# Kernel optimization log

Hardware: AMD Instinct MI355X
Metric: run time of the kernel (lower is better)

Reference implementation:

```python
import jax, jax.numpy as jnp
import numpy as np

V_PATCH = (1, 2, 4, 8, 16, 32)
RESI = 0.5   # abs(quant_resi)
BETA = 0.25
K_PHI = 4    # share_quant_resi


def _phi_idx(si, SN, K=K_PHI):
    # PhiPartiallyShared.__getitem__ with at = si/(SN-1)
    ticks = np.linspace(1/3/K, 1 - 1/3/K, K) if K == 4 else np.linspace(1/2/K, 1 - 1/2/K, K)
    return int(np.argmin(np.abs(ticks - si / (SN - 1))))


def _area_down(x, pn):
    # F.interpolate mode='area' with pn | H  == exact block mean
    B, C, H, W = x.shape
    return x.reshape(B, C, pn, H // pn, pn, W // pn).mean(axis=(3, 5))


def _bilinear(x, size):
    # matches torch bilinear, align_corners=False, antialias=False (half-pixel centers)
    B, C, _, _ = x.shape
    return jax.image.resize(x, (B, C, size, size), method='bilinear', antialias=False)


def _down(x, pn, si):
    if pn == x.shape[2]:
        return x
    return _area_down(x, pn) if si <= 3 else _bilinear(x, pn)


def _phi_ada(h, w, b, fw, fb, sn):
    # Phi_ada: conv weight modulated by fc(SN); fc is zero-init but kept in the graph
    C = h.shape[1]
    cond = (fw[:, 0] * jnp.float32(sn) + fb).reshape(C, C, 1, 1)
    wmod = w * (1.0 + cond)
    y = jax.lax.conv_general_dilated(h, wmod, (1, 1), 'SAME',
                                     dimension_numbers=('NCHW', 'OIHW', 'NCHW'))
    y = y + b[None, :, None, None]
    return h * (1.0 - RESI) + y * RESI


def _forward(f, embed_w, conv_w, conv_b, fc_w, fc_b):
    B, C, H, W = f.shape
    SN = len(V_PATCH)
    f_ng = jax.lax.stop_gradient(f)
    f_rest = f_ng
    f_hat = jnp.zeros_like(f_ng)
    e_ng = jax.lax.stop_gradient(embed_w)            # embedding.weight.data
    e_sq = jnp.sum(e_ng * e_ng, axis=1)              # [V]
    vq_losses = []
    commit = jnp.float32(0.0)
    for si, pn in enumerate(V_PATCH):
        rest = f_rest if si == SN - 1 else _down(f_rest, pn, si)
        rest_NC = rest.transpose(0, 2, 3, 1).reshape(-1, C)          # [N,C]
        # squared L2 distances to codebook, argmin (non-differentiable)
        d = (jnp.sum(rest_NC * rest_NC, axis=1, keepdims=True)
             + e_sq - 2.0 * (rest_NC @ e_ng.T))                       # [N,V]
        idx = jnp.argmin(d, axis=1)                                   # [N]
        h = embed_w[idx].reshape(B, pn, pn, C).transpose(0, 3, 1, 2)  # [B,C,pn,pn]
        if si != SN - 1:
            h = _bilinear(h, H)
        k = _phi_idx(si, SN)
        h = _phi_ada(h, conv_w[k], conv_b[k], fc_w[k], fc_b[k], SN)
        f_hat = f_hat + h
        f_rest = f_rest - jax.lax.stop_gradient(h)    # grad through f_rest is killed by argmin anyway
        vq_losses.append(jnp.mean((f_hat - f_ng) ** 2))
        fh_ng = jax.lax.stop_gradient(f_hat)
        commit = commit + jnp.mean((_down(fh_ng, pn, si) - _down(f, pn, si)) ** 2) * BETA
    commit = commit / SN
    # straight-through estimator
    f_hat_out = jax.lax.stop_gradient(f_hat) - f_ng + f
    return f_hat_out, jnp.stack(vq_losses), commit


def setup_inputs() -> dict:
    key = jax.random.key(0)
    k1, k2, k3 = jax.random.split(key, 3)
    B, C, H, W = 32, 64, 32, 32
    V = 4096
    f_BChw = jax.random.normal(k1, (B, C, H, W), dtype=jnp.float32)
    embed_w = jax.random.normal(k2, (V, C), dtype=jnp.float32) * 0.5  # trunc_normal std=0.5
    conv_w = jax.random.normal(k3, (K_PHI, C, C, 3, 3), dtype=jnp.float32) * 0.02
    conv_b = jnp.zeros((K_PHI, C), dtype=jnp.float32)
    fc_w = jnp.zeros((K_PHI, C * C, 1), dtype=jnp.float32)  # Phi_ada.fc zero-init
    fc_b = jnp.zeros((K_PHI, C * C), dtype=jnp.float32)
    return {'f_BChw': f_BChw, 'embed_w': embed_w, 'conv_w': conv_w,
            'conv_b': conv_b, 'fc_w': fc_w, 'fc_b': fc_b}


def reference(f_BChw, embed_w, conv_w, conv_b, fc_w, fc_b):
    return _forward(f_BChw, embed_w, conv_w, conv_b, fc_w, fc_b)
```

## Files before the change

### kernel.cpp

```cpp
#include <hip/hip_runtime.h>
#include <cfloat>

#define N_ELEM 2097152
#define TAU 2.0e-2f

typedef short s16x8 __attribute__((ext_vector_type(8)));
typedef float f32x4 __attribute__((ext_vector_type(4)));

__device__ __forceinline__ unsigned short f2bf(float v) {
    unsigned u = __float_as_uint(v);
    u += 0x7FFFu + ((u >> 16) & 1u);
    return (unsigned short)(u >> 16);
}
__device__ __forceinline__ float bf2f(unsigned short h) {
    return __uint_as_float(((unsigned)h) << 16);
}

__device__ __forceinline__ float blockReduceSum(float v) {
    __shared__ float red[4];
    #pragma unroll
    for (int off = 32; off; off >>= 1) v += __shfl_down(v, off, 64);
    int wid = threadIdx.x >> 6, lane = threadIdx.x & 63;
    if (lane == 0) red[wid] = v;
    __syncthreads();
    float r = 0.f;
    if (threadIdx.x == 0) {
        int nw = ((int)blockDim.x + 63) >> 6;
        for (int w = 0; w < nw; ++w) r += red[w];
    }
    __syncthreads();
    return r;
}

__global__ void k_embprep(const float* __restrict__ e, float* __restrict__ hesq,
                          unsigned short* __restrict__ ehiN, unsigned short* __restrict__ eloN) {
    int v = blockIdx.x * 256 + threadIdx.x;
    if (v >= 4096) return;
    const float4* r = (const float4*)(e + (size_t)v * 64);
    float s = 0.f;
    #pragma unroll
    for (int i = 0; i < 16; ++i) {
        float4 a = r[i];
        s += a.x * a.x + a.y * a.y + a.z * a.z + a.w * a.w;
    }
    hesq[v] = 0.5f * s;
    for (int i = 0; i < 64; ++i) {
        float x = e[(size_t)v * 64 + i];
        unsigned short h = f2bf(x);
        ehiN[(size_t)v * 64 + i] = h ^ 0x8000u;
        eloN[(size_t)v * 64 + i] = f2bf(x - bf2f(h)) ^ 0x8000u;
    }
}

__global__ void k_wmod(const float* __restrict__ w, const float* __restrict__ fcw,
                       const float* __restrict__ fcb,
                       unsigned short* __restrict__ wh, unsigned short* __restrict__ wl) {
    int i = blockIdx.x * 256 + threadIdx.x;
    if (i >= 4 * 64 * 64 * 9) return;
    int k = i / (64 * 64 * 9);
    int r = i % (64 * 64 * 9);
    int oi = r / 9;
    int t = r % 9;
    int co = oi >> 6, ci = oi & 63;
    float cond = fcw[k * 4096 + oi] * 6.0f + fcb[k * 4096 + oi];
    float v = w[i] * (1.0f + cond);
    size_t o = ((size_t)(k * 9 + t) * 64 + co) * 64 + ci;
    unsigned short h = f2bf(v);
    wh[o] = h;
    wl[o] = f2bf(v - bf2f(h));
}

__global__ __launch_bounds__(256) void k_down_plane(
        const float* __restrict__ f, const float* __restrict__ fhat,
        float* __restrict__ restnc, unsigned short* __restrict__ dhi,
        unsigned short* __restrict__ dlo, float* __restrict__ cmpPrev, int pn) {
    __shared__ float hs[32][16];
    __shared__ float cr[32][16];
    __shared__ float pm[256];
    int bc = blockIdx.x;
    int c = bc & 63, b = bc >> 6;
    int t = threadIdx.x;
    const float4* fp = (const float4*)(f + (size_t)bc * 1024);
    const float4* hp = (const float4*)(fhat + (size_t)bc * 1024);
    float4 a = fp[t], q = hp[t];
    int r = t >> 3, c4 = t & 7;
    hs[r][c4 * 2]     = (a.x - q.x) + (a.y - q.y);
    hs[r][c4 * 2 + 1] = (a.z - q.z) + (a.w - q.w);
    __syncthreads();
    int cpp = 16 / pn;
    for (int i = t; i < 32 * pn; i += 256) {
        int rr = i / pn, px = i % pn;
        float s = 0.f;
        for (int j = 0; j < cpp; ++j) s += hs[rr][px * cpp + j];
        cr[rr][px] = s;
    }
    __syncthreads();
    int s_ = 32 / pn;
    float inv = 1.0f / (float)(s_ * s_);
    for (int p = t; p < pn * pn; p += 256) {
        int py = p / pn, px = p % pn;
        float s = 0.f;
        for (int j = 0; j < s_; ++j) s += cr[py * s_ + j][px];
        float m = s * inv;
        pm[p] = m;
        int n = (b * pn + py) * pn + px;
        size_t o = (size_t)n * 64 + c;
        unsigned short h = f2bf(m);
        restnc[o] = m;
        dhi[o] = h;
        dlo[o] = f2bf(m - bf2f(h));
    }
    if (pn >= 2) {
        __syncthreads();
        int pnp = pn >> 1;
        float m2 = 0.f;
        for (int p = t; p < pnp * pnp; p += 256) {
            int py = p / pnp, px = p % pnp;
            float mm = 0.25f * (pm[(2 * py) * pn + 2 * px] + pm[(2 * py) * pn + 2 * px + 1]
                              + pm[(2 * py + 1) * pn + 2 * px] + pm[(2 * py + 1) * pn + 2 * px + 1]);
            m2 += mm * mm;
        }
        m2 = blockReduceSum(m2);
        if (t == 0) cmpPrev[blockIdx.x] = m2;
    }
}

__global__ void k_trans_nc(const float* __restrict__ A, const float* __restrict__ Bt,
                           float* __restrict__ dst,
                           unsigned short* __restrict__ dhi, unsigned short* __restrict__ dlo) {
    __shared__ float t[64][65];
    int b = blockIdx.x;
    int p0 = blockIdx.y * 64;
    int lane = threadIdx.x & 63, r4 = threadIdx.x >> 6;
    #pragma unroll
    for (int i = 0; i < 16; ++i) {
        int c = i * 4 + r4;
        size_t g = ((size_t)b * 64 + c) * 1024 + p0 + lane;
        t[c][lane] = A[g] - Bt[g];
    }
    __syncthreads();
    #pragma unroll
    for (int i = 0; i < 16; ++i) {
        int p = i * 4 + r4;
        size_t o = ((size_t)(b * 1024 + p0 + p)) * 64 + lane;
        float v = t[lane][p];
        unsigned short h = f2bf(v);
        dst[o] = v;
        dhi[o] = h;
        dlo[o] = f2bf(v - bf2f(h));
    }
}

__global__ __launch_bounds__(256) void k_commit_rest(const float* __restrict__ restnc,
                                                     float* __restrict__ cmp) {
    int i = blockIdx.x * 256 + threadIdx.x;
    int c = i & 63;
    int p = i >> 6;
    int px = p & 15; p >>= 4;
    int py = p & 15; p >>= 4;
    int b = p;
    int n00 = (b * 32 + 2 * py) * 32 + 2 * px;
    float m = 0.25f * (restnc[(size_t)n00 * 64 + c] + restnc[(size_t)(n00 + 1) * 64 + c]
                     + restnc[(size_t)(n00 + 32) * 64 + c] + restnc[(size_t)(n00 + 33) * 64 + c]);
    float m2 = blockReduceSum(m * m);
    if (threadIdx.x == 0) cmp[blockIdx.x] = m2;
}

__global__ __launch_bounds__(256) void k_vq_mfma(
        const unsigned short* __restrict__ resthi, const unsigned short* __restrict__ restlo,
        const unsigned short* __restrict__ embhiN, const unsigned short* __restrict__ embloN,
        const float* __restrict__ hesq,
        float* __restrict__ m1v_, int* __restrict__ m1i_, float* __restrict__ m2v_,
        int N, int CPS) {
    __shared__ __align__(16) unsigned short lah[64 * 64];
    __shared__ __align__(16) unsigned short lal[64 * 64];
    __shared__ __align__(16) float lq[64];
    int tid = threadIdx.x;
    int lane = tid & 63, wv = tid >> 6;
    int split = blockIdx.y;
    int p0 = blockIdx.x * 128 + wv * 32;
    int cr = lane & 15, oct = lane >> 4;
    int ko8 = oct * 8;
    int ptA = p0 + cr, ptB = p0 + 16 + cr;
    int pA = min(ptA, N - 1), pB = min(ptB, N - 1);

    const unsigned short* ra = resthi + (size_t)pA * 64;
    const unsigned short* la = restlo + (size_t)pA * 64;
    const unsigned short* rb = resthi + (size_t)pB * 64;
    const unsigned short* lb = restlo + (size_t)pB * 64;
    s16x8 bhA0 = *(const s16x8*)(ra + ko8);
    s16x8 bhA1 = *(const s16x8*)(ra + 32 + ko8);
    s16x8 blA0 = *(const s16x8*)(la + ko8);
    s16x8 blA1 = *(const s16x8*)(la + 32 + ko8);
    s16x8 bhB0 = *(const s16x8*)(rb + ko8);
    s16x8 bhB1 = *(const s16x8*)(rb + 32 + ko8);
    s16x8 blB0 = *(const s16x8*)(lb + ko8);
    s16x8 blB1 = *(const s16x8*)(lb + 32 + ko8);

    float m1vA = FLT_MAX, m2vA = FLT_MAX; int m1iA = 0;
    float m1vB = FLT_MAX, m2vB = FLT_MAX; int m1iB = 0;

    int cbeg = split * CPS;
    for (int oc = 0; oc < CPS; oc += 64) {
        int cb = cbeg + oc;
        __syncthreads();
        for (int t = tid; t < 512; t += 256) {
            int cc = t >> 3, part = t & 7;
            int bo = (cc * 128 + part * 16) ^ ((cc & 7) << 4);
            *(uint4*)((char*)lah + bo) = *(const uint4*)(embhiN + (size_t)(cb + cc) * 64 + part * 8);
            *(uint4*)((char*)lal + bo) = *(const uint4*)(embloN + (size_t)(cb + cc) * 64 + part * 8);
        }
        if (tid < 64) lq[tid] = hesq[cb + tid];
        __syncthreads();
        #pragma unroll
        for (int sub = 0; sub < 4; ++sub) {
            int cl = sub * 16 + cr;
            int sw = (cl & 7) << 4;
            int rowb = cl * 128;
            s16x8 ah0 = *(const s16x8*)((const char*)lah + ((rowb + ko8 * 2) ^ sw));
            s16x8 ah1 = *(const s16x8*)((const char*)lah + ((rowb + 64 + ko8 * 2) ^ sw));
            s16x8 al0 = *(const s16x8*)((const char*)lal + ((rowb + ko8 * 2) ^ sw));
            s16x8 al1 = *(const s16x8*)((const char*)lal + ((rowb + 64 + ko8 * 2) ^ sw));
            f32x4 q = *(const f32x4*)(lq + sub * 16 + oct * 4);
            int crow = cb + sub * 16 + oct * 4;
            f32x4 acc = q;
            acc = __builtin_amdgcn_mfma_f32_16x16x32_bf16(ah0, bhA0, acc, 0, 0, 0);
            acc = __builtin_amdgcn_mfma_f32_16x16x32_bf16(ah1, bhA1, acc, 0, 0, 0);
            acc = __builtin_amdgcn_mfma_f32_16x16x32_bf16(ah0, blA0, acc, 0, 0, 0);
            acc = __builtin_amdgcn_mfma_f32_16x16x32_bf16(ah1, blA1, acc, 0, 0, 0);
            acc = __builtin_amdgcn_mfma_f32_16x16x32_bf16(al0, bhA0, acc, 0, 0, 0);
            acc = __builtin_amdgcn_mfma_f32_16x16x32_bf16(al1, bhA1, acc, 0, 0, 0);
            #pragma unroll
            for (int r = 0; r < 4; ++r) {
                float s = acc[r]; int c = crow + r;
                bool lt1 = s < m1vA, lt2 = s < m2vA;
                float nm2 = lt2 ? s : m2vA;
                m2vA = lt1 ? m1vA : nm2;
                m1iA = lt1 ? c : m1iA;
                m1vA = lt1 ? s : m1vA;
            }
            f32x4 accB = q;
            accB = __builtin_amdgcn_mfma_f32_16x16x32_bf16(ah0, bhB0, accB, 0, 0, 0);
            accB = __builtin_amdgcn_mfma_f32_16x16x32_bf16(ah1, bhB1, accB, 0, 0, 0);
            accB = __builtin_amdgcn_mfma_f32_16x16x32_bf16(ah0, blB0, accB, 0, 0, 0);
            accB = __builtin_amdgcn_mfma_f32_16x16x32_bf16(ah1, blB1, accB, 0, 0, 0);
            accB = __builtin_amdgcn_mfma_f32_16x16x32_bf16(al0, bhB0, accB, 0, 0, 0);
            accB = __builtin_amdgcn_mfma_f32_16x16x32_bf16(al1, bhB1, accB, 0, 0, 0);
            #pragma unroll
            for (int r = 0; r < 4; ++r) {
                float s = accB[r]; int c = crow + r;
                bool lt1 = s < m1vB, lt2 = s < m2vB;
                float nm2 = lt2 ? s : m2vB;
                m2vB = lt1 ? m1vB : nm2;
                m1iB = lt1 ? c : m1iB;
                m1vB = lt1 ? s : m1vB;
            }
        }
    }
    #pragma unroll
    for (int off = 16; off <= 32; off <<= 1) {
        float o1 = __shfl_xor(m1vA, off, 64); int oi = __shfl_xor(m1iA, off, 64);
        float o2 = __shfl_xor(m2vA, off, 64);
        if (o1 < m1vA) { m2vA = fminf(m1vA, o2); m1vA = o1; m1iA = oi; }
        else if (o1 < m2vA) m2vA = o1;
        o1 = __shfl_xor(m1vB, off, 64); oi = __shfl_xor(m1iB, off, 64);
        o2 = __shfl_xor(m2vB, off, 64);
        if (o1 < m1vB) { m2vB = fminf(m1vB, o2); m1vB = o1; m1iB = oi; }
        else if (o1 < m2vB) m2vB = o1;
    }
    if (oct == 0) {
        if (ptA < N) { size_t o = (size_t)split * N + ptA; m1v_[o] = m1vA; m1i_[o] = m1iA; m2v_[o] = m2vA; }
        if (ptB < N) { size_t o = (size_t)split * N + ptB; m1v_[o] = m1vB; m1i_[o] = m1iB; m2v_[o] = m2vB; }
    }
}

__global__ void k_vq_combine(const float* __restrict__ m1v_, const int* __restrict__ m1i_,
                             const float* __restrict__ m2v_,
                             int* __restrict__ idx, int* __restrict__ flag, int* __restrict__ count,
                             unsigned long long* __restrict__ pmin, int N, int SPLITS) {
    int n = blockIdx.x * 256 + threadIdx.x;
    if (n >= N) return;
    float a1v = m1v_[n], a2v = m2v_[n];
    int a1i = m1i_[n];
    for (int s = 1; s < SPLITS; ++s) {
        size_t o = (size_t)s * N + n;
        float b1v = m1v_[o], b2v = m2v_[o];
        int b1i = m1i_[o];
        if (b1v < a1v) {
            a2v = fminf(a1v, b2v);
            a1v = b1v; a1i = b1i;
        } else if (b1v < a2v) {
            a2v = b1v;
        }
    }
    idx[n] = a1i;
    pmin[n] = 0xFFFFFFFFFFFFFFFFull;
    if (a2v - a1v < TAU) {
        int p = atomicAdd(count, 1);
        flag[p] = n;
    }
}

__global__ __launch_bounds__(256) void k_vq_exact(
        const float* __restrict__ restnc, const float* __restrict__ embed,
        const float* __restrict__ hesq, const int* __restrict__ flag,
        const int* __restrict__ count, unsigned long long* __restrict__ pmin) {
    __shared__ float rs[32 * 64];
    int tid = threadIdx.x;
    int lane = tid & 63;
    int cnt = *count;
    int nb = (cnt + 31) >> 5;
    int ntask = nb * 16;
    for (int task = blockIdx.x; task < ntask; task += gridDim.x) {
        int batch = task >> 4, spl = task & 15;
        int lbase = batch << 5;
        int npts = min(32, cnt - lbase);
        __syncthreads();
        for (int i = tid; i < npts * 64; i += 256) {
            int li = i >> 6;
            rs[i] = restnc[(size_t)flag[lbase + li] * 64 + (i & 63)];
        }
        __syncthreads();
        int code = spl * 256 + tid;
        const float4* e4 = (const float4*)(embed + (size_t)code * 64);
        float4 e[16];
        #pragma unroll
        for (int i = 0; i < 16; ++i) e[i] = e4[i];
        float hq = hesq[code];
        for (int p = 0; p < npts; ++p) {
            const float4* r4 = (const float4*)(rs + p * 64);
            float d0 = 0.f, d1 = 0.f, d2 = 0.f, d3 = 0.f;
            #pragma unroll
            for (int i = 0; i < 16; i += 4) {
                float4 e0 = e[i], e1 = e[i + 1], e2 = e[i + 2], e3 = e[i + 3];
                d0 += e0.x * r4[i].x     + e0.y * r4[i].y     + e0.z * r4[i].z     + e0.w * r4[i].w;
                d1 += e1.x * r4[i + 1].x + e1.y * r4[i + 1].y + e1.z * r4[i + 1].z + e1.w * r4[i + 1].w;
                d2 += e2.x * r4[i + 2].x + e2.y * r4[i + 2].y + e2.z * r4[i + 2].z + e2.w * r4[i + 2].w;
                d3 += e3.x * r4[i + 3].x + e3.y * r4[i + 3].y + e3.z * r4[i + 3].z + e3.w * r4[i + 3].w;
            }
            float s = hq - ((d0 + d1) + (d2 + d3));
            unsigned u = __float_as_uint(s);
            u = (u & 0x80000000u) ? ~u : (u | 0x80000000u);
            unsigned long long pk = (((unsigned long long)u) << 32) | (unsigned)code;
            #pragma unroll
            for (int off = 32; off; off >>= 1) {
                unsigned long long o = __shfl_down(pk, off, 64);
                if (o < pk) pk = o;
            }
            if (lane == 0) atomicMin(pmin + flag[lbase + p], pk);
        }
    }
}

__global__ void k_up(const int* __restrict__ idx, const unsigned long long* __restrict__ pmin,
                     const float* __restrict__ embed, float* __restrict__ hupf,
                     unsigned short* __restrict__ huph, unsigned short* __restrict__ hupl,
                     int pn) {
    int i = blockIdx.x * 256 + threadIdx.x;
    if (i >= N_ELEM) return;
    int c = i & 63, x = (i >> 6) & 31, y = (i >> 11) & 31, b = i >> 16;
    float v;
    if (pn == 32) {
        int n = (b * 32 + y) * 32 + x;
        unsigned long long pv = pmin[n];
        int id = (pv != 0xFFFFFFFFFFFFFFFFull) ? (int)(pv & 0xFFFFFFFFull) : idx[n];
        v = embed[(size_t)id * 64 + c];
    } else {
        float scale = (float)pn * (1.0f / 32.0f);
        float sy = (y + 0.5f) * scale - 0.5f;
        float sx = (x + 0.5f) * scale - 0.5f;
        float fy0 = floorf(sy), fx0 = floorf(sx);
        float wy = sy - fy0, wx = sx - fx0;
        int y0 = max(0, min(pn - 1, (int)fy0));
        int y1 = max(0, min(pn - 1, (int)fy0 + 1));
        int x0 = max(0, min(pn - 1, (int)fx0));
        int x1 = max(0, min(pn - 1, (int)fx0 + 1));
        int nb_ = b * pn * pn;
        int n00 = nb_ + y0 * pn + x0, n01 = nb_ + y0 * pn + x1;
        int n10 = nb_ + y1 * pn + x0, n11 = nb_ + y1 * pn + x1;
        unsigned long long p00 = pmin[n00], p01 = pmin[n01], p10 = pmin[n10], p11 = pmin[n11];
        int i00 = (p00 != 0xFFFFFFFFFFFFFFFFull) ? (int)(p00 & 0xFFFFFFFFull) : idx[n00];
        int i01 = (p01 != 0xFFFFFFFFFFFFFFFFull) ? (int)(p01 & 0xFFFFFFFFull) : idx[n01];
        int i10 = (p10 != 0xFFFFFFFFFFFFFFFFull) ? (int)(p10 & 0xFFFFFFFFull) : idx[n10];
        int i11 = (p11 != 0xFFFFFFFFFFFFFFFFull) ? (int)(p11 & 0xFFFFFFFFull) : idx[n11];
        float v00 = embed[(size_t)i00 * 64 + c];
        float v01 = embed[(size_t)i01 * 64 + c];
        float v10 = embed[(size_t)i10 * 64 + c];
        float v11 = embed[(size_t)i11 * 64 + c];
        v = (1.f - wy) * ((1.f - wx) * v00 + wx * v01) + wy * ((1.f - wx) * v10 + wx * v11);
    }
    hupf[i] = v;
    unsigned short h = f2bf(v);
    huph[i] = h;
    hupl[i] = f2bf(v - bf2f(h));
}

__global__ __launch_bounds__(256) void k_conv_mfma(
        const unsigned short* __restrict__ huph, const unsigned short* __restrict__ hupl,
        const float* __restrict__ hupf,
        const unsigned short* __restrict__ wh, const unsigned short* __restrict__ wl,
        const float* __restrict__ bias, const float* __restrict__ f_in,
        float* __restrict__ f_hat, float* __restrict__ vq_part) {
    __shared__ __align__(16) unsigned short Xh[6 * 34 * 64];
    __shared__ __align__(16) unsigned short Xl[6 * 34 * 64];
    int b = blockIdx.x, rg = blockIdx.y;
    int y0 = rg * 4;
    int tid = threadIdx.x;
    int lane = tid & 63, wv = tid >> 6;
    int co0 = wv * 16;
    int cr = lane & 15, oct = lane >> 4;

    for (int q = tid; q < 6 * 34 * 8; q += 256) {
        int pl = q >> 3, o8 = q & 7;
        int lr = pl / 34, lc = pl % 34;
        int gy = y0 + lr - 1, gx = lc - 1;
        int bo = (pl * 128 + o8 * 16) ^ ((lc & 7) << 4);
        uint4 vh = {0, 0, 0, 0}, vl = {0, 0, 0, 0};
        if (gy >= 0 && gy < 32 && gx >= 0 && gx < 32) {
            size_t g = (((size_t)(b * 32 + gy)) * 32 + gx) * 64 + o8 * 8;
            vh = *(const uint4*)(huph + g);
            vl = *(const uint4*)(hupl + g);
        }
        *(uint4*)((char*)Xh + bo) = vh;
        *(uint4*)((char*)Xl + bo) = vl;
    }
    __syncthreads();

    f32x4 acc[8];
    #pragma unroll
    for (int ps = 0; ps < 8; ++ps) acc[ps] = (f32x4){0.f, 0.f, 0.f, 0.f};

    for (int t = 0; t < 9; ++t) {
        int dy = t / 3, dx = t % 3;
        #pragma unroll
        for (int cc = 0; cc < 2; ++cc) {
            size_t wo = ((size_t)t * 64 + co0 + cr) * 64 + cc * 32 + oct * 8;
            s16x8 Ah = *(const s16x8*)(wh + wo);
            s16x8 Al = *(const s16x8*)(wl + wo);
            #pragma unroll
            for (int ps = 0; ps < 8; ++ps) {
                int px = ps * 16 + cr;
                int lr = (px >> 5) + dy;
                int lc = (px & 31) + dx;
                int bo = ((lr * 34 + lc) * 128 + cc * 64 + oct * 16) ^ ((lc & 7) << 4);
                s16x8 Bh = *(const s16x8*)((const char*)Xh + bo);
                s16x8 Bl = *(const s16x8*)((const char*)Xl + bo);
                acc[ps] = __builtin_amdgcn_mfma_f32_16x16x32_bf16(Ah, Bh, acc[ps], 0, 0, 0);
                acc[ps] = __builtin_amdgcn_mfma_f32_16x16x32_bf16(Ah, Bl, acc[ps], 0, 0, 0);
                acc[ps] = __builtin_amdgcn_mfma_f32_16x16x32_bf16(Al, Bh, acc[ps], 0, 0, 0);
                acc[ps] = __builtin_amdgcn_mfma_f32_16x16x32_bf16(Al, Bl, acc[ps], 0, 0, 0);
            }
        }
    }

    const float* hupb = hupf + (size_t)b * 65536;
    float local = 0.f;
    #pragma unroll
    for (int ps = 0; ps < 8; ++ps) {
        int px = ps * 16 + cr;
        int y = y0 + (px >> 5), x = px & 31;
        #pragma unroll
        for (int r = 0; r < 4; ++r) {
            int co = co0 + oct * 4 + r;
            float hv = hupb[(size_t)(y * 32 + x) * 64 + co];
            float hconv = acc[ps][r] + bias[co];
            float hout = 0.5f * hv + 0.5f * hconv;
            size_t o = (((size_t)(b * 64 + co)) * 32 + y) * 32 + x;
            float fh = f_hat[o] + hout;
            f_hat[o] = fh;
            float d = fh - f_in[o];
            local += d * d;
        }
    }
    local = blockReduceSum(local);
    if (tid == 0) vq_part[b * 8 + rg] = local;
}

__global__ void k_final(const float* __restrict__ vqp, const float* __restrict__ cmpP,
                        float* __restrict__ out) {
    const int pn2s[5] = {1, 4, 16, 64, 256};
    __shared__ float commit_s;
    if (threadIdx.x == 0) commit_s = 0.f;
    __syncthreads();
    for (int si = 0; si < 6; ++si) {
        float l = vqp[si * 256 + threadIdx.x];
        l = blockReduceSum(l);
        if (threadIdx.x == 0) {
            float vl = l / (float)N_ELEM;
            out[N_ELEM + si] = vl;
            if (si == 5) commit_s += vl * 0.25f;
        }
        if (si < 5) {
            float csum = 0.f;
            for (int i = threadIdx.x; i < 2048; i += 256) csum += cmpP[si * 2048 + i];
            csum = blockReduceSum(csum);
            if (threadIdx.x == 0) commit_s += csum / (float)(2048 * pn2s[si]) * 0.25f;
        }
    }
    __syncthreads();
    if (threadIdx.x == 0) out[N_ELEM + 6] = commit_s / 6.0f;
}

extern "C" void kernel_launch(void* const* d_in, const int* in_sizes, int n_in,
                              void* d_out, int out_size, void* d_ws, size_t ws_size,
                              hipStream_t stream) {
    const float* f     = (const float*)d_in[0];
    const float* embed = (const float*)d_in[1];
    const float* convw = (const float*)d_in[2];
    const float* convb = (const float*)d_in[3];
    const float* fcw   = (const float*)d_in[4];
    const float* fcb   = (const float*)d_in[5];
    float* out = (float*)d_out;
    float* ws  = (float*)d_ws;

    float* hupf   = ws;
    float* restnc = ws + 2097152;
    unsigned short* resthi = (unsigned short*)(ws + 4194304);
    unsigned short* restlo = (unsigned short*)(ws + 5242880);
    unsigned short* huph   = resthi;
    unsigned short* hupl   = restlo;
    unsigned short* embhiN = (unsigned short*)(ws + 6291456);
    unsigned short* embloN = (unsigned short*)(ws + 6422528);
    unsigned short* wmodh  = (unsigned short*)(ws + 6553600);
    unsigned short* wmodl  = (unsigned short*)(ws + 6627328);
    float* hesq   = ws + 6701056;
    float* m1v    = ws + 6705152;
    float* m2v    = ws + 6836224;
    int*   m1i    = (int*)(ws + 6967296);
    int*   idx    = (int*)(ws + 7098368);
    int*   flag   = (int*)(ws + 7131136);
    int*   count  = (int*)(ws + 7163904);
    unsigned long long* pmin = (unsigned long long*)(ws + 7163968);
    float* vqp    = ws + 7229504;
    float* cmpP   = ws + 7231040;

    hipMemsetAsync(d_out, 0, (size_t)out_size * sizeof(float), stream);
    hipMemsetAsync(count, 0, 6 * sizeof(int), stream);
    k_wmod<<<576, 256, 0, stream>>>(convw, fcw, fcb, wmodh, wmodl);
    k_embprep<<<16, 256, 0, stream>>>(embed, hesq, embhiN, embloN);

    const int pns[6]    = {1, 2, 4, 8, 16, 32};
    const int splits[6] = {64, 64, 32, 16, 8, 4};
    const int kidx[6]   = {0, 0, 1, 2, 3, 3};

    for (int si = 0; si < 6; ++si) {
        int pn = pns[si], pn2 = pn * pn;
        int N = 32 * pn2, SPL = splits[si], CPS = 4096 / SPL;

        if (si <= 4) {
            k_down_plane<<<2048, 256, 0, stream>>>(f, out, restnc, resthi, restlo,
                                                   si >= 1 ? cmpP + (si - 1) * 2048 : nullptr, pn);
        } else {
            k_trans_nc<<<dim3(32, 16), 256, 0, stream>>>(f, out, restnc, resthi, restlo);
            k_commit_rest<<<2048, 256, 0, stream>>>(restnc, cmpP + 4 * 2048);
        }

        k_vq_mfma<<<dim3((N + 127) / 128, SPL), 256, 0, stream>>>(resthi, restlo, embhiN, embloN, hesq,
                                                                  m1v, m1i, m2v, N, CPS);
        k_vq_combine<<<(N + 255) / 256, 256, 0, stream>>>(m1v, m1i, m2v, idx, flag, count + si, pmin, N, SPL);
        k_vq_exact<<<512, 256, 0, stream>>>(restnc, embed, hesq, flag, count + si, pmin);

        k_up<<<(N_ELEM + 255) / 256, 256, 0, stream>>>(idx, pmin, embed, hupf, huph, hupl, pn);

        k_conv_mfma<<<dim3(32, 8), 256, 0, stream>>>(huph, hupl, hupf,
                                                     wmodh + kidx[si] * 36864, wmodl + kidx[si] * 36864,
                                                     convb + kidx[si] * 64, f, out, vqp + si * 256);
    }

    k_final<<<1, 256, 0, stream>>>(vqp, cmpP, out);
}
```

Before: 627.6 us.

## Retile conv MFMA, drop fp32 upsample buffer, branchless top-2 min tracking

The conv kernel now gives each wave a 32-channel by 4-pixel-tile block instead of 16 channels by 8 tiles, so each LDS B fragment feeds two output-channel tiles. It also drops the low*low MFMA term. The fp32 upsampled buffer is removed: the residual h value is rebuilt from the hi/lo bf16 halves already in LDS, which cuts a 8 MB global write and read per scale. Top-2 distance tracking in the VQ kernels becomes branchless min/max, and the swizzle term is hoisted out of the loop. Risks are a small precision loss from the dropped lo*lo product and from the bf16 hi+lo reconstruction.

```diff
diff --git a/kernel.cpp b/kernel.cpp
--- a/kernel.cpp
+++ b/kernel.cpp
@@ -199,6 +199,7 @@
 
     float m1vA = FLT_MAX, m2vA = FLT_MAX; int m1iA = 0;
     float m1vB = FLT_MAX, m2vB = FLT_MAX; int m1iB = 0;
+    int sw = (cr & 7) << 4;
 
     int cbeg = split * CPS;
     for (int oc = 0; oc < CPS; oc += 64) {
@@ -214,9 +215,7 @@
         __syncthreads();
         #pragma unroll
         for (int sub = 0; sub < 4; ++sub) {
-            int cl = sub * 16 + cr;
-            int sw = (cl & 7) << 4;
-            int rowb = cl * 128;
+            int rowb = (sub * 16 + cr) * 128;
             s16x8 ah0 = *(const s16x8*)((const char*)lah + ((rowb + ko8 * 2) ^ sw));
             s16x8 ah1 = *(const s16x8*)((const char*)lah + ((rowb + 64 + ko8 * 2) ^ sw));
             s16x8 al0 = *(const s16x8*)((const char*)lal + ((rowb + ko8 * 2) ^ sw));
@@ -232,12 +231,11 @@
             acc = __builtin_amdgcn_mfma_f32_16x16x32_bf16(al1, bhA1, acc, 0, 0, 0);
             #pragma unroll
             for (int r = 0; r < 4; ++r) {
-                float s = acc[r]; int c = crow + r;
-                bool lt1 = s < m1vA, lt2 = s < m2vA;
-                float nm2 = lt2 ? s : m2vA;
-                m2vA = lt1 ? m1vA : nm2;
-                m1iA = lt1 ? c : m1iA;
-                m1vA = lt1 ? s : m1vA;
+                float s = acc[r];
+                bool lt = s < m1vA;
+                m2vA = fminf(fmaxf(s, m1vA), m2vA);
+                m1iA = lt ? (crow + r) : m1iA;
+                m1vA = fminf(s, m1vA);
             }
             f32x4 accB = q;
             accB = __builtin_amdgcn_mfma_f32_16x16x32_bf16(ah0, bhB0, accB, 0, 0, 0);
@@ -248,12 +246,11 @@
             accB = __builtin_amdgcn_mfma_f32_16x16x32_bf16(al1, bhB1, accB, 0, 0, 0);
             #pragma unroll
             for (int r = 0; r < 4; ++r) {
-                float s = accB[r]; int c = crow + r;
-                bool lt1 = s < m1vB, lt2 = s < m2vB;
-                float nm2 = lt2 ? s : m2vB;
-                m2vB = lt1 ? m1vB : nm2;
-                m1iB = lt1 ? c : m1iB;
-                m1vB = lt1 ? s : m1vB;
+                float s = accB[r];
+                bool lt = s < m1vB;
+                m2vB = fminf(fmaxf(s, m1vB), m2vB);
+                m1iB = lt ? (crow + r) : m1iB;
+                m1vB = fminf(s, m1vB);
             }
         }
     }
@@ -261,12 +258,16 @@
     for (int off = 16; off <= 32; off <<= 1) {
         float o1 = __shfl_xor(m1vA, off, 64); int oi = __shfl_xor(m1iA, off, 64);
         float o2 = __shfl_xor(m2vA, off, 64);
-        if (o1 < m1vA) { m2vA = fminf(m1vA, o2); m1vA = o1; m1iA = oi; }
-        else if (o1 < m2vA) m2vA = o1;
+        bool lt = o1 < m1vA;
+        m2vA = fminf(fmaxf(o1, m1vA), fminf(m2vA, o2));
+        m1vA = fminf(o1, m1vA);
+        m1iA = lt ? oi : m1iA;
         o1 = __shfl_xor(m1vB, off, 64); oi = __shfl_xor(m1iB, off, 64);
         o2 = __shfl_xor(m2vB, off, 64);
-        if (o1 < m1vB) { m2vB = fminf(m1vB, o2); m1vB = o1; m1iB = oi; }
-        else if (o1 < m2vB) m2vB = o1;
+        lt = o1 < m1vB;
+        m2vB = fminf(fmaxf(o1, m1vB), fminf(m2vB, o2));
+        m1vB = fminf(o1, m1vB);
+        m1iB = lt ? oi : m1iB;
     }
     if (oct == 0) {
         if (ptA < N) { size_t o = (size_t)split * N + ptA; m1v_[o] = m1vA; m1i_[o] = m1iA; m2v_[o] = m2vA; }
@@ -286,12 +287,10 @@
         size_t o = (size_t)s * N + n;
         float b1v = m1v_[o], b2v = m2v_[o];
         int b1i = m1i_[o];
-        if (b1v < a1v) {
-            a2v = fminf(a1v, b2v);
-            a1v = b1v; a1i = b1i;
-        } else if (b1v < a2v) {
-            a2v = b1v;
-        }
+        bool lt = b1v < a1v;
+        a2v = fminf(fmaxf(b1v, a1v), fminf(a2v, b2v));
+        a1v = fminf(b1v, a1v);
+        a1i = lt ? b1i : a1i;
     }
     idx[n] = a1i;
     pmin[n] = 0xFFFFFFFFFFFFFFFFull;
@@ -353,7 +352,7 @@
 }
 
 __global__ void k_up(const int* __restrict__ idx, const unsigned long long* __restrict__ pmin,
-                     const float* __restrict__ embed, float* __restrict__ hupf,
+                     const float* __restrict__ embed,
                      unsigned short* __restrict__ huph, unsigned short* __restrict__ hupl,
                      int pn) {
     int i = blockIdx.x * 256 + threadIdx.x;
@@ -389,7 +388,6 @@
         float v11 = embed[(size_t)i11 * 64 + c];
         v = (1.f - wy) * ((1.f - wx) * v00 + wx * v01) + wy * ((1.f - wx) * v10 + wx * v11);
     }
-    hupf[i] = v;
     unsigned short h = f2bf(v);
     huph[i] = h;
     hupl[i] = f2bf(v - bf2f(h));
@@ -397,7 +395,6 @@
 
 __global__ __launch_bounds__(256) void k_conv_mfma(
         const unsigned short* __restrict__ huph, const unsigned short* __restrict__ hupl,
-        const float* __restrict__ hupf,
         const unsigned short* __restrict__ wh, const unsigned short* __restrict__ wl,
         const float* __restrict__ bias, const float* __restrict__ f_in,
         float* __restrict__ f_hat, float* __restrict__ vq_part) {
@@ -407,7 +404,8 @@
     int y0 = rg * 4;
     int tid = threadIdx.x;
     int lane = tid & 63, wv = tid >> 6;
-    int co0 = wv * 16;
+    int coh = (wv & 1) * 32;
+    int ph  = (wv >> 1) * 4;
     int cr = lane & 15, oct = lane >> 4;
 
     for (int q = tid; q < 6 * 34 * 8; q += 256) {
@@ -426,50 +424,66 @@
     }
     __syncthreads();
 
-    f32x4 acc[8];
-    #pragma unroll
-    for (int ps = 0; ps < 8; ++ps) acc[ps] = (f32x4){0.f, 0.f, 0.f, 0.f};
+    f32x4 acc[2][4];
+    #pragma unroll
+    for (int ct = 0; ct < 2; ++ct)
+        #pragma unroll
+        for (int pp = 0; pp < 4; ++pp) acc[ct][pp] = (f32x4){0.f, 0.f, 0.f, 0.f};
 
     for (int t = 0; t < 9; ++t) {
         int dy = t / 3, dx = t % 3;
         #pragma unroll
         for (int cc = 0; cc < 2; ++cc) {
-            size_t wo = ((size_t)t * 64 + co0 + cr) * 64 + cc * 32 + oct * 8;
-            s16x8 Ah = *(const s16x8*)(wh + wo);
-            s16x8 Al = *(const s16x8*)(wl + wo);
+            size_t wo0 = ((size_t)t * 64 + coh + cr) * 64 + cc * 32 + oct * 8;
+            size_t wo1 = ((size_t)t * 64 + coh + 16 + cr) * 64 + cc * 32 + oct * 8;
+            s16x8 Ah0 = *(const s16x8*)(wh + wo0);
+            s16x8 Al0 = *(const s16x8*)(wl + wo0);
+            s16x8 Ah1 = *(const s16x8*)(wh + wo1);
+            s16x8 Al1 = *(const s16x8*)(wl + wo1);
             #pragma unroll
-            for (int ps = 0; ps < 8; ++ps) {
-                int px = ps * 16 + cr;
+            for (int pp = 0; pp < 4; ++pp) {
+                int px = (ph + pp) * 16 + cr;
                 int lr = (px >> 5) + dy;
                 int lc = (px & 31) + dx;
                 int bo = ((lr * 34 + lc) * 128 + cc * 64 + oct * 16) ^ ((lc & 7) << 4);
                 s16x8 Bh = *(const s16x8*)((const char*)Xh + bo);
                 s16x8 Bl = *(const s16x8*)((const char*)Xl + bo);
-                acc[ps] = __builtin_amdgcn_mfma_f32_16x16x32_bf16(Ah, Bh, acc[ps], 0, 0, 0);
-                acc[ps] = __builtin_amdgcn_mfma_f32_16x16x32_bf16(Ah, Bl, acc[ps], 0, 0, 0);
-                acc[ps] = __builtin_amdgcn_mfma_f32_16x16x32_bf16(Al, Bh, acc[ps], 0, 0, 0);
-                acc[ps] = __builtin_amdgcn_mfma_f32_16x16x32_bf16(Al, Bl, acc[ps], 0, 0, 0);
+                acc[0][pp] = __builtin_amdgcn_mfma_f32_16x16x32_bf16(Ah0, Bh, acc[0][pp], 0, 0, 0);
+                acc[0][pp] = __builtin_amdgcn_mfma_f32_16x16x32_bf16(Ah0, Bl, acc[0][pp], 0, 0, 0);
+                acc[0][pp] = __builtin_amdgcn_mfma_f32_16x16x32_bf16(Al0, Bh, acc[0][pp], 0, 0, 0);
+                acc[1][pp] = __builtin_amdgcn_mfma_f32_16x16x32_bf16(Ah1, Bh, acc[1][pp], 0, 0, 0);
+                acc[1][pp] = __builtin_amdgcn_mfma_f32_16x16x32_bf16(Ah1, Bl, acc[1][pp], 0, 0, 0);
+                acc[1][pp] = __builtin_amdgcn_mfma_f32_16x16x32_bf16(Al1, Bh, acc[1][pp], 0, 0, 0);
             }
         }
     }
 
-    const float* hupb = hupf + (size_t)b * 65536;
     float local = 0.f;
     #pragma unroll
-    for (int ps = 0; ps < 8; ++ps) {
-        int px = ps * 16 + cr;
-        int y = y0 + (px >> 5), x = px & 31;
+    for (int ct = 0; ct < 2; ++ct) {
+        int cbase = coh + ct * 16 + oct * 4;
         #pragma unroll
-        for (int r = 0; r < 4; ++r) {
-            int co = co0 + oct * 4 + r;
-            float hv = hupb[(size_t)(y * 32 + x) * 64 + co];
-            float hconv = acc[ps][r] + bias[co];
-            float hout = 0.5f * hv + 0.5f * hconv;
-            size_t o = (((size_t)(b * 64 + co)) * 32 + y) * 32 + x;
-            float fh = f_hat[o] + hout;
-            f_hat[o] = fh;
-            float d = fh - f_in[o];
-            local += d * d;
+        for (int pp = 0; pp < 4; ++pp) {
+            int px = (ph + pp) * 16 + cr;
+            int y = y0 + (px >> 5), x = px & 31;
+            int lr = (px >> 5) + 1, lc = (px & 31) + 1;
+            int bo = ((lr * 34 + lc) * 128 + cbase * 2) ^ ((lc & 7) << 4);
+            ushort4 hvh = *(const ushort4*)((const char*)Xh + bo);
+            ushort4 hvl = *(const ushort4*)((const char*)Xl + bo);
+            #pragma unroll
+            for (int r = 0; r < 4; ++r) {
+                int co = cbase + r;
+                unsigned short uh = (r == 0) ? hvh.x : (r == 1) ? hvh.y : (r == 2) ? hvh.z : hvh.w;
+                unsigned short ul = (r == 0) ? hvl.x : (r == 1) ? hvl.y : (r == 2) ? hvl.z : hvl.w;
+                float hv = bf2f(uh) + bf2f(ul);
+                float hconv = acc[ct][pp][r] + bias[co];
+                float hout = 0.5f * hv + 0.5f * hconv;
+                size_t o = (((size_t)(b * 64 + co)) * 32 + y) * 32 + x;
+                float fh = f_hat[o] + hout;
+                f_hat[o] = fh;
+                float d = fh - f_in[o];
+                local += d * d;
+            }
         }
     }
     local = blockReduceSum(local);
@@ -513,7 +527,6 @@
     float* out = (float*)d_out;
     float* ws  = (float*)d_ws;
 
-    float* hupf   = ws;
     float* restnc = ws + 2097152;
     unsigned short* resthi = (unsigned short*)(ws + 4194304);
     unsigned short* restlo = (unsigned short*)(ws + 5242880);
@@ -560,9 +573,9 @@
         k_vq_combine<<<(N + 255) / 256, 256, 0, stream>>>(m1v, m1i, m2v, idx, flag, count + si, pmin, N, SPL);
         k_vq_exact<<<512, 256, 0, stream>>>(restnc, embed, hesq, flag, count + si, pmin);
 
-        k_up<<<(N_ELEM + 255) / 256, 256, 0, stream>>>(idx, pmin, embed, hupf, huph, hupl, pn);
-
-        k_conv_mfma<<<dim3(32, 8), 256, 0, stream>>>(huph, hupl, hupf,
+        k_up<<<(N_ELEM + 255) / 256, 256, 0, stream>>>(idx, pmin, embed, huph, hupl, pn);
+
+        k_conv_mfma<<<dim3(32, 8), 256, 0, stream>>>(huph, hupl,
                                                      wmodh + kidx[si] * 36864, wmodl + kidx[si] * 36864,
                                                      convb + kidx[si] * 64, f, out, vqp + si * 256);
     }
```

After: 595.8 us. -5.1%, faster.
